# Optimization experiments

Hardware: AMD Instinct MI355X
Metric: run time of the kernel (lower is better)

## Reference

```python
import jax, jax.numpy as jnp
import numpy as np

N_NODES = 100000
N_EDGES = 3200000
IN_DIM = 512
HID = 256


def setup_inputs() -> dict:
    key = jax.random.key(0)
    ks = jax.random.split(key, 12)
    s1 = 1.0 / np.sqrt(HID)
    s2 = 1.0 / np.sqrt(HID)
    return {
        "inputs": jax.random.normal(ks[0], (N_NODES, IN_DIM), dtype=jnp.float32),
        "edge_rows": jax.random.randint(ks[1], (N_EDGES,), 0, N_NODES, dtype=jnp.int32),
        "edge_cols": jax.random.randint(ks[2], (N_EDGES,), 0, N_NODES, dtype=jnp.int32),
        "edge_vals": jax.random.uniform(ks[3], (N_EDGES,), dtype=jnp.float32),
        "W1": jax.random.uniform(ks[4], (IN_DIM, HID), minval=-s1, maxval=s1, dtype=jnp.float32),
        "b1": jax.random.uniform(ks[5], (HID,), minval=-s1, maxval=s1, dtype=jnp.float32),
        "W2": jax.random.uniform(ks[6], (HID, HID), minval=-s2, maxval=s2, dtype=jnp.float32),
        "b2": jax.random.uniform(ks[7], (HID,), minval=-s2, maxval=s2, dtype=jnp.float32),
        "fc1_W": jax.random.normal(ks[8], (HID, 32), dtype=jnp.float32) * 0.06,
        "fc1_b": jnp.zeros((32,), dtype=jnp.float32),
        "fc2_W": jax.random.normal(ks[9], (32, 2), dtype=jnp.float32) * 0.18,
        "fc2_b": jnp.zeros((2,), dtype=jnp.float32),
    }


def _spmm(rows, cols, vals, dense):
    # sparse[N,N] @ dense[N,D]: gather source rows, scale, scatter-add to dest rows
    gathered = dense[cols] * vals[:, None]          # [E, D]
    return jax.ops.segment_sum(gathered, rows, num_segments=N_NODES)


def _gcn_layer(x, rows, cols, vals, W, b):
    support = x @ W                                  # [N, out]
    return _spmm(rows, cols, vals, support) + b


def reference(inputs, edge_rows, edge_cols, edge_vals, W1, b1, W2, b2,
              fc1_W, fc1_b, fc2_W, fc2_b):
    h = jax.nn.relu(_gcn_layer(inputs, edge_rows, edge_cols, edge_vals, W1, b1))
    logits = _gcn_layer(h, edge_rows, edge_cols, edge_vals, W2, b2)
    h_a = jax.nn.relu(logits @ fc1_W + fc1_b)        # [N, 32]
    return jax.nn.log_softmax(h_a @ fc2_W + fc2_b, axis=1)  # [N, 2]
```

## Files before the change

kernel.cpp:

```cpp
#include <hip/hip_runtime.h>
#include <hip/hip_bf16.h>
#include <math.h>

#define N_NODES 100000
#define N_EDGES 3200000
#define IN_DIM  512
#define HID     256

#define NBUK    1021
#define ROWS_PBK 98
#define BCAPG   4096
#define CHUNK   4096
#define WFT_S   260

typedef __attribute__((ext_vector_type(8))) _Float16 f16x8;
typedef __attribute__((ext_vector_type(2))) _Float16 h2v;
typedef __attribute__((ext_vector_type(4))) float f32x4;

__device__ __forceinline__ ushort f2h(float f) {
  return __builtin_bit_cast(ushort, (_Float16)f);
}
__device__ __forceinline__ float hlo(uint u) {
  return (float)__builtin_bit_cast(h2v, u).x;
}
__device__ __forceinline__ float hhi(uint u) {
  return (float)__builtin_bit_cast(h2v, u).y;
}

__global__ __launch_bounds__(256) void fuse_weights(
    const float* __restrict__ W2, const float* __restrict__ fc1W,
    const float* __restrict__ b2, const float* __restrict__ fc1b,
    ushort* __restrict__ WfTb, float* __restrict__ bf,
    int* __restrict__ gcur) {
  int tid = threadIdx.x;
  int i = blockIdx.x * 32 + (tid >> 3);
  int jg = (tid & 7) * 4;
  float4 acc = {0.f, 0.f, 0.f, 0.f};
  for (int k = 0; k < HID; k++) {
    float w = W2[i * HID + k];
    float4 f = *(const float4*)(fc1W + k * 32 + jg);
    acc.x += w * f.x; acc.y += w * f.y; acc.z += w * f.z; acc.w += w * f.w;
  }
  WfTb[(jg + 0) * HID + i] = f2h(acc.x);
  WfTb[(jg + 1) * HID + i] = f2h(acc.y);
  WfTb[(jg + 2) * HID + i] = f2h(acc.z);
  WfTb[(jg + 3) * HID + i] = f2h(acc.w);
  if (blockIdx.x == 0 && tid < 32) {
    float s = fc1b[tid];
    for (int k = 0; k < HID; k++) s += b2[k] * fc1W[k * 32 + tid];
    bf[tid] = s;
  }
  int gid = blockIdx.x * 256 + tid;
  if (gid < NBUK) gcur[gid] = gid * BCAPG;
}

__global__ __launch_bounds__(256) void prep_w1t(
    const float* __restrict__ W1, ushort* __restrict__ W1T) {
  int n = blockIdx.x;
  for (int k = threadIdx.x; k < IN_DIM; k += 256)
    W1T[(size_t)n * IN_DIM + k] = f2h(W1[(size_t)k * HID + n]);
}

__global__ __launch_bounds__(256) void blocksum_kernel(
    const int* __restrict__ cnt, int* __restrict__ bsum, int n) {
  int i = blockIdx.x * 256 + threadIdx.x;
  int v = (i < n) ? cnt[i] : 0;
  #pragma unroll
  for (int m = 1; m < 64; m <<= 1) v += __shfl_xor(v, m, 64);
  __shared__ int ws[4];
  if ((threadIdx.x & 63) == 0) ws[threadIdx.x >> 6] = v;
  __syncthreads();
  if (threadIdx.x == 0) bsum[blockIdx.x] = ws[0] + ws[1] + ws[2] + ws[3];
}

__global__ __launch_bounds__(512) void scanpart_kernel(
    int* __restrict__ bsum, int nb) {
  int tid = threadIdx.x, lane = tid & 63, wid = tid >> 6;
  int v = (tid < nb) ? bsum[tid] : 0;
  int x = v;
  #pragma unroll
  for (int d = 1; d < 64; d <<= 1) {
    int y = __shfl_up(x, d, 64);
    if (lane >= d) x += y;
  }
  __shared__ int ws[8];
  if (lane == 63) ws[wid] = x;
  __syncthreads();
  int woff = 0;
  for (int w = 0; w < wid; w++) woff += ws[w];
  if (tid < nb) bsum[tid] = woff + x - v;
}

__global__ __launch_bounds__(256) void scanfinal_kernel(
    const int* __restrict__ cnt, const int* __restrict__ bsum,
    int* __restrict__ rowptr, int n) {
  int tid = threadIdx.x, lane = tid & 63, wid = tid >> 6;
  int i = blockIdx.x * 256 + tid;
  int v = (i < n) ? cnt[i] : 0;
  int x = v;
  #pragma unroll
  for (int d = 1; d < 64; d <<= 1) {
    int y = __shfl_up(x, d, 64);
    if (lane >= d) x += y;
  }
  __shared__ int ws[4];
  if (lane == 63) ws[wid] = x;
  __syncthreads();
  int woff = bsum[blockIdx.x];
  for (int w = 0; w < wid; w++) woff += ws[w];
  int excl = woff + x - v;
  if (i < n) rowptr[i] = excl;
  if (i == 0) rowptr[n] = N_EDGES;
}

__global__ __launch_bounds__(256) void scatter_p1(
    const int* __restrict__ rows, const int* __restrict__ cols,
    const float* __restrict__ vals, int* __restrict__ gcur,
    int2* __restrict__ tcv, int* __restrict__ cnt, int n) {
  __shared__ int bcnt[NBUK];
  __shared__ int bcur[NBUK];
  int tid = threadIdx.x;
  int chunk0 = blockIdx.x * CHUNK;
  for (int i = tid; i < NBUK; i += 256) bcnt[i] = 0;
  __syncthreads();

  int r[16], c[16], b[16];
  float v[16];
  #pragma unroll
  for (int i = 0; i < 16; i++) {
    int idx = chunk0 + i * 256 + tid;
    if (idx < n) {
      r[i] = rows[idx];
      c[i] = cols[idx];
      v[i] = vals[idx];
      b[i] = r[i] / ROWS_PBK;
      atomicAdd(&bcnt[b[i]], 1);
      atomicAdd(&cnt[r[i]], 1);
    } else {
      b[i] = -1;
    }
  }
  __syncthreads();
  for (int i = tid; i < NBUK; i += 256)
    if (bcnt[i] > 0) bcur[i] = atomicAdd(&gcur[i], bcnt[i]);
  __syncthreads();
  #pragma unroll
  for (int i = 0; i < 16; i++) {
    if (b[i] >= 0) {
      int p = atomicAdd(&bcur[b[i]], 1);
      int rl = r[i] - b[i] * ROWS_PBK;
      int2 e; e.x = (rl << 17) | c[i]; e.y = __float_as_int(v[i]);
      tcv[p] = e;
    }
  }
}

__global__ __launch_bounds__(256) void scatter_p2(
    const int* __restrict__ rowptr, const int2* __restrict__ tcv,
    int2* __restrict__ cv) {
  __shared__ int2 buf[BCAPG];
  __shared__ int lcur[ROWS_PBK];
  int b = blockIdx.x;
  int tid = threadIdx.x;
  int lo = b * ROWS_PBK;
  int hi = min(N_NODES, lo + ROWS_PBK);
  int nr = hi - lo;
  int base = rowptr[lo];
  int ecnt = rowptr[hi] - base;
  for (int r = tid; r < nr; r += 256) lcur[r] = rowptr[lo + r] - base;
  __syncthreads();
  const int2* src = tcv + (size_t)b * BCAPG;
  for (int i = tid; i < ecnt; i += 256) {
    int2 e = src[i];
    int rl = ((uint)e.x) >> 17;
    int p = atomicAdd(&lcur[rl], 1);
    int2 o; o.x = e.x & 0x1FFFF; o.y = e.y;
    buf[p] = o;
  }
  __syncthreads();
  int2* dst = cv + base;
  for (int i = tid; i < ecnt; i += 256) dst[i] = buf[i];
}

__global__ __launch_bounds__(512, 4) void gemm1_mfma(
    const float* __restrict__ A, const ushort* __restrict__ BT,
    ushort* __restrict__ C, int M) {
  __shared__ __align__(16) char smem[32768];
  ushort* As = (ushort*)smem;
  ushort* Bs = (ushort*)(smem + 10240);
  int tid = threadIdx.x;
  int bm = blockIdx.x * 128;
  int lane = tid & 63, wid = tid >> 6;
  int waveM = wid >> 2, waveN = wid & 3;
  int l16 = lane & 15, quad = lane >> 4;

  f32x4 acc[4][4] = {};

  int ar = tid >> 2;
  int ac = (tid & 3) * 8;
  const float* aptr = A + (size_t)(bm + ar) * IN_DIM + ac;
  bool avalid = (bm + ar) < M;
  ushort* aw = As + ar * 40 + ac;
  int br = tid >> 1;
  int bc = (tid & 1) * 16;
  const ushort* bptr = BT + (size_t)br * IN_DIM + bc;
  ushort* bw = Bs + br * 40 + bc;

  for (int k0 = 0; k0 < IN_DIM; k0 += 32) {
    #pragma unroll
    for (int i = 0; i < 2; i++) {
      float4 av = {0.f, 0.f, 0.f, 0.f};
      if (avalid) av = *(const float4*)(aptr + k0 + i * 4);
      ushort4 p;
      p.x = f2h(av.x); p.y = f2h(av.y); p.z = f2h(av.z); p.w = f2h(av.w);
      *(ushort4*)(aw + i * 4) = p;
    }
    *(int4*)bw = *(const int4*)(bptr + k0);
    *(int4*)(bw + 8) = *(const int4*)(bptr + k0 + 8);
    __syncthreads();

    f16x8 af[4], bfv[4];
    #pragma unroll
    for (int mi = 0; mi < 4; mi++)
      af[mi] = *(const f16x8*)(As + (waveM * 64 + mi * 16 + l16) * 40 + quad * 8);
    #pragma unroll
    for (int ni = 0; ni < 4; ni++)
      bfv[ni] = *(const f16x8*)(Bs + (waveN * 64 + ni * 16 + l16) * 40 + quad * 8);
    #pragma unroll
    for (int mi = 0; mi < 4; mi++)
      #pragma unroll
      for (int ni = 0; ni < 4; ni++)
        acc[mi][ni] = __builtin_amdgcn_mfma_f32_16x16x32_f16(
            af[mi], bfv[ni], acc[mi][ni], 0, 0, 0);
    __syncthreads();
  }

  ushort* Cs = (ushort*)smem;
  #pragma unroll
  for (int wm = 0; wm < 2; wm++) {
    if (waveM == wm) {
      #pragma unroll
      for (int mi = 0; mi < 4; mi++)
        #pragma unroll
        for (int ni = 0; ni < 4; ni++)
          #pragma unroll
          for (int r = 0; r < 4; r++)
            Cs[(mi * 16 + quad * 4 + r) * 256 + waveN * 64 + ni * 16 + l16] =
                f2h(acc[mi][ni][r]);
    }
    __syncthreads();
    int rbase = bm + wm * 64;
    #pragma unroll
    for (int i = 0; i < 4; i++) {
      int f = tid + i * 512;
      int r = f >> 5, v8 = f & 31;
      if (rbase + r < M)
        *(int4*)(C + (size_t)(rbase + r) * HID + v8 * 8) =
            *(const int4*)(Cs + r * 256 + v8 * 8);
    }
    __syncthreads();
  }
}

__global__ __launch_bounds__(512, 8) void spmm_fused(
    const int* __restrict__ rowptr, const int2* __restrict__ cv,
    const ushort* __restrict__ S, const float* __restrict__ bias,
    const ushort* __restrict__ WfTb, ushort* __restrict__ S2b, int nrows) {
  __shared__ ushort WfT[32 * WFT_S];
  __shared__ float hbuf[8][256];
  int tid = threadIdx.x;
  for (int idx = tid; idx < 32 * 64; idx += 512) {
    int jj = idx >> 6, kg = idx & 63;
    *(ushort4*)&WfT[jj * WFT_S + kg * 4] = *(const ushort4*)&WfTb[jj * HID + kg * 4];
  }
  __syncthreads();

  int w = tid >> 6, lane = tid & 63;
  int row = blockIdx.x * 8 + w;
  if (row >= nrows) return;
  int start = rowptr[row], end = rowptr[row + 1];
  float A0 = 0.f, A1 = 0.f, A2 = 0.f, A3 = 0.f;
  const ushort* Sl = S + lane * 4;
  int j = start;
  if ((j & 1) && j < end) {
    int2 e0 = cv[j];
    float v0 = __int_as_float(e0.y);
    uint2 u0 = *(const uint2*)(Sl + (size_t)e0.x * HID);
    A0 += v0 * hlo(u0.x); A1 += v0 * hhi(u0.x);
    A2 += v0 * hlo(u0.y); A3 += v0 * hhi(u0.y);
    j++;
  }
  for (; j + 7 < end; j += 8) {
    int4 E[4];
    #pragma unroll
    for (int t = 0; t < 4; t++)
      E[t] = *(const int4*)((const int*)(cv + j) + t * 4);
    uint2 u[8];
    #pragma unroll
    for (int t = 0; t < 4; t++) {
      u[2 * t]     = *(const uint2*)(Sl + (size_t)E[t].x * HID);
      u[2 * t + 1] = *(const uint2*)(Sl + (size_t)E[t].z * HID);
    }
    #pragma unroll
    for (int t = 0; t < 4; t++) {
      float va = __int_as_float(E[t].y);
      float vb = __int_as_float(E[t].w);
      A0 += va * hlo(u[2 * t].x);     A1 += va * hhi(u[2 * t].x);
      A2 += va * hlo(u[2 * t].y);     A3 += va * hhi(u[2 * t].y);
      A0 += vb * hlo(u[2 * t + 1].x); A1 += vb * hhi(u[2 * t + 1].x);
      A2 += vb * hlo(u[2 * t + 1].y); A3 += vb * hhi(u[2 * t + 1].y);
    }
  }
  for (; j + 1 < end; j += 2) {
    int4 E = *(const int4*)(cv + j);
    uint2 ua = *(const uint2*)(Sl + (size_t)E.x * HID);
    uint2 ub = *(const uint2*)(Sl + (size_t)E.z * HID);
    float va = __int_as_float(E.y), vb = __int_as_float(E.w);
    A0 += va * hlo(ua.x); A1 += va * hhi(ua.x);
    A2 += va * hlo(ua.y); A3 += va * hhi(ua.y);
    A0 += vb * hlo(ub.x); A1 += vb * hhi(ub.x);
    A2 += vb * hlo(ub.y); A3 += vb * hhi(ub.y);
  }
  if (j < end) {
    int2 e0 = cv[j];
    float v0 = __int_as_float(e0.y);
    uint2 u0 = *(const uint2*)(Sl + (size_t)e0.x * HID);
    A0 += v0 * hlo(u0.x); A1 += v0 * hhi(u0.x);
    A2 += v0 * hlo(u0.y); A3 += v0 * hhi(u0.y);
  }
  float4 b = *(const float4*)(bias + lane * 4);
  float4 h;
  h.x = fmaxf(A0 + b.x, 0.f);
  h.y = fmaxf(A1 + b.y, 0.f);
  h.z = fmaxf(A2 + b.z, 0.f);
  h.w = fmaxf(A3 + b.w, 0.f);
  *(float4*)(&hbuf[w][lane * 4]) = h;

  int jo = lane & 31;
  int kbase = (lane >> 5) * 128;
  const float* hb = &hbuf[w][kbase];
  const ushort* wt = &WfT[jo * WFT_S + kbase];
  float c0 = 0.f, c1 = 0.f, c2 = 0.f, c3 = 0.f;
  #pragma unroll
  for (int kk = 0; kk < 32; kk++) {
    float4 hv = *(const float4*)(hb + kk * 4);
    uint2 wv = *(const uint2*)(wt + kk * 4);
    c0 += hv.x * hlo(wv.x); c1 += hv.y * hhi(wv.x);
    c2 += hv.z * hlo(wv.y); c3 += hv.w * hhi(wv.y);
  }
  float acc = (c0 + c1) + (c2 + c3);
  acc += __shfl_xor(acc, 32, 64);
  if (lane < 32) S2b[(size_t)row * 32 + jo] = f2h(acc);
}

__global__ __launch_bounds__(256) void spmm32_out_kernel(
    const int* __restrict__ rowptr, const int2* __restrict__ cv,
    const ushort* __restrict__ S2b, const float* __restrict__ bf,
    const float* __restrict__ fc2W, const float* __restrict__ fc2b,
    float* __restrict__ out, int nrows) {
  int sub = threadIdx.x >> 4;
  int l16 = threadIdx.x & 15;
  int row = blockIdx.x * 16 + sub;
  if (row >= nrows) return;
  int start = rowptr[row], end = rowptr[row + 1];
  float a0 = 0.f, a1 = 0.f;
  const ushort* Sl = S2b + l16 * 2;
  int j = start;
  if ((j & 1) && j < end) {
    int2 e0 = cv[j];
    float v0 = __int_as_float(e0.y);
    uint u0 = *(const uint*)(Sl + (size_t)e0.x * 32);
    a0 += v0 * hlo(u0); a1 += v0 * hhi(u0);
    j++;
  }
  for (; j + 15 < end; j += 16) {
    int4 E[8];
    #pragma unroll
    for (int t = 0; t < 8; t++)
      E[t] = *(const int4*)((const int*)(cv + j) + t * 4);
    uint u[16];
    #pragma unroll
    for (int t = 0; t < 8; t++) {
      u[2 * t]     = *(const uint*)(Sl + (size_t)E[t].x * 32);
      u[2 * t + 1] = *(const uint*)(Sl + (size_t)E[t].z * 32);
    }
    #pragma unroll
    for (int t = 0; t < 8; t++) {
      float va = __int_as_float(E[t].y);
      float vb = __int_as_float(E[t].w);
      a0 += va * hlo(u[2 * t]);     a1 += va * hhi(u[2 * t]);
      a0 += vb * hlo(u[2 * t + 1]); a1 += vb * hhi(u[2 * t + 1]);
    }
  }
  for (; j + 1 < end; j += 2) {
    int4 E = *(const int4*)(cv + j);
    uint ua = *(const uint*)(Sl + (size_t)E.x * 32);
    uint ub = *(const uint*)(Sl + (size_t)E.z * 32);
    float va = __int_as_float(E.y), vb = __int_as_float(E.w);
    a0 += va * hlo(ua); a1 += va * hhi(ua);
    a0 += vb * hlo(ub); a1 += vb * hhi(ub);
  }
  if (j < end) {
    int2 e0 = cv[j];
    float v0 = __int_as_float(e0.y);
    uint u0 = *(const uint*)(Sl + (size_t)e0.x * 32);
    a0 += v0 * hlo(u0); a1 += v0 * hhi(u0);
  }
  int k0 = l16 * 2, k1 = l16 * 2 + 1;
  float h0 = fmaxf(a0 + bf[k0], 0.f);
  float h1 = fmaxf(a1 + bf[k1], 0.f);
  float z0p = h0 * fc2W[k0 * 2 + 0] + h1 * fc2W[k1 * 2 + 0];
  float z1p = h0 * fc2W[k0 * 2 + 1] + h1 * fc2W[k1 * 2 + 1];
  #pragma unroll
  for (int m = 8; m >= 1; m >>= 1) {
    z0p += __shfl_xor(z0p, m, 16);
    z1p += __shfl_xor(z1p, m, 16);
  }
  if (l16 == 0) {
    float z0 = z0p + fc2b[0];
    float z1 = z1p + fc2b[1];
    float mx = fmaxf(z0, z1);
    float lse = mx + logf(expf(z0 - mx) + expf(z1 - mx));
    float2 o = {z0 - lse, z1 - lse};
    *(float2*)(out + (size_t)row * 2) = o;
  }
}

extern "C" void kernel_launch(void* const* d_in, const int* in_sizes, int n_in,
                              void* d_out, int out_size, void* d_ws, size_t ws_size,
                              hipStream_t stream) {
  const float* X     = (const float*)d_in[0];
  const int*   erow  = (const int*)d_in[1];
  const int*   ecol  = (const int*)d_in[2];
  const float* eval_ = (const float*)d_in[3];
  const float* W1    = (const float*)d_in[4];
  const float* b1    = (const float*)d_in[5];
  const float* W2    = (const float*)d_in[6];
  const float* b2    = (const float*)d_in[7];
  const float* fc1W  = (const float*)d_in[8];
  const float* fc1b  = (const float*)d_in[9];
  const float* fc2W  = (const float*)d_in[10];
  const float* fc2b  = (const float*)d_in[11];
  float* out = (float*)d_out;

  size_t off = 0;
  auto alloc = [&](size_t bytes) {
    void* p = (char*)d_ws + off;
    off += (bytes + 255) & ~(size_t)255;
    return p;
  };
  ushort* WfTb   = (ushort*)alloc((size_t)HID * 32 * 2);
  float*  bf     = (float*)alloc(32 * 4);
  int*    cnt    = (int*)alloc((size_t)N_NODES * 4);
  int*    rowptr = (int*)alloc((size_t)(N_NODES + 1) * 4);
  int*    bsum   = (int*)alloc((size_t)512 * 4);
  int*    gcur   = (int*)alloc((size_t)NBUK * 4);
  int2*   cv     = (int2*)alloc((size_t)N_EDGES * 8);
  int2*   tcv    = (int2*)alloc((size_t)NBUK * BCAPG * 8);
  ushort* W1T    = (ushort*)alloc((size_t)HID * IN_DIM * 2);
  ushort* S1b    = (ushort*)alloc((size_t)N_NODES * HID * 2);
  ushort* S2b    = (ushort*)alloc((size_t)N_NODES * 32 * 2);
  (void)ws_size; (void)n_in; (void)in_sizes; (void)out_size;

  const int NBLK = (N_NODES + 255) / 256;
  const int NCHUNK = (N_EDGES + CHUNK - 1) / CHUNK;

  hipMemsetAsync(cnt, 0, (size_t)N_NODES * 4, stream);

  fuse_weights<<<8, 256, 0, stream>>>(W2, fc1W, b2, fc1b, WfTb, bf, gcur);
  prep_w1t<<<HID, 256, 0, stream>>>(W1, W1T);

  scatter_p1<<<NCHUNK, 256, 0, stream>>>(
      erow, ecol, eval_, gcur, tcv, cnt, N_EDGES);
  blocksum_kernel<<<NBLK, 256, 0, stream>>>(cnt, bsum, N_NODES);
  scanpart_kernel<<<1, 512, 0, stream>>>(bsum, NBLK);
  scanfinal_kernel<<<NBLK, 256, 0, stream>>>(cnt, bsum, rowptr, N_NODES);
  scatter_p2<<<NBUK, 256, 0, stream>>>(rowptr, tcv, cv);

  gemm1_mfma<<<(N_NODES + 127) / 128, 512, 0, stream>>>(X, W1T, S1b, N_NODES);

  spmm_fused<<<(N_NODES + 7) / 8, 512, 0, stream>>>(
      rowptr, cv, S1b, b1, WfTb, S2b, N_NODES);

  spmm32_out_kernel<<<(N_NODES + 15) / 16, 256, 0, stream>>>(
      rowptr, cv, S2b, bf, fc2W, fc2b, out, N_NODES);
}
```

Before: 812.1 us.

## Derive CSR rowptr from bucket counts, drop global per-row count atomics and scans

Stops counting edges per row with global atomics in scatter_p1. Row offsets are now computed from per-bucket totals: a single-block scan over the 1021 buckets, then a per-bucket count-and-scan in shared memory inside scatter_p2. This removes the memset, the 3.2M global atomics and three scan kernels, in exchange for an extra pass over the bucket's edges in scatter_p2. It also splits spmm_fused into two launches over row halves, which adds a launch and has no clear speed purpose.

```diff
diff --git a/kernel.cpp b/kernel.cpp
--- a/kernel.cpp
+++ b/kernel.cpp
@@ -12,6 +12,7 @@
 #define BCAPG   4096
 #define CHUNK   4096
 #define WFT_S   260
+#define SPMM_HALF 50000
 
 typedef __attribute__((ext_vector_type(8))) _Float16 f16x8;
 typedef __attribute__((ext_vector_type(2))) _Float16 h2v;
@@ -61,62 +62,10 @@
     W1T[(size_t)n * IN_DIM + k] = f2h(W1[(size_t)k * HID + n]);
 }
 
-__global__ __launch_bounds__(256) void blocksum_kernel(
-    const int* __restrict__ cnt, int* __restrict__ bsum, int n) {
-  int i = blockIdx.x * 256 + threadIdx.x;
-  int v = (i < n) ? cnt[i] : 0;
-  #pragma unroll
-  for (int m = 1; m < 64; m <<= 1) v += __shfl_xor(v, m, 64);
-  __shared__ int ws[4];
-  if ((threadIdx.x & 63) == 0) ws[threadIdx.x >> 6] = v;
-  __syncthreads();
-  if (threadIdx.x == 0) bsum[blockIdx.x] = ws[0] + ws[1] + ws[2] + ws[3];
-}
-
-__global__ __launch_bounds__(512) void scanpart_kernel(
-    int* __restrict__ bsum, int nb) {
-  int tid = threadIdx.x, lane = tid & 63, wid = tid >> 6;
-  int v = (tid < nb) ? bsum[tid] : 0;
-  int x = v;
-  #pragma unroll
-  for (int d = 1; d < 64; d <<= 1) {
-    int y = __shfl_up(x, d, 64);
-    if (lane >= d) x += y;
-  }
-  __shared__ int ws[8];
-  if (lane == 63) ws[wid] = x;
-  __syncthreads();
-  int woff = 0;
-  for (int w = 0; w < wid; w++) woff += ws[w];
-  if (tid < nb) bsum[tid] = woff + x - v;
-}
-
-__global__ __launch_bounds__(256) void scanfinal_kernel(
-    const int* __restrict__ cnt, const int* __restrict__ bsum,
-    int* __restrict__ rowptr, int n) {
-  int tid = threadIdx.x, lane = tid & 63, wid = tid >> 6;
-  int i = blockIdx.x * 256 + tid;
-  int v = (i < n) ? cnt[i] : 0;
-  int x = v;
-  #pragma unroll
-  for (int d = 1; d < 64; d <<= 1) {
-    int y = __shfl_up(x, d, 64);
-    if (lane >= d) x += y;
-  }
-  __shared__ int ws[4];
-  if (lane == 63) ws[wid] = x;
-  __syncthreads();
-  int woff = bsum[blockIdx.x];
-  for (int w = 0; w < wid; w++) woff += ws[w];
-  int excl = woff + x - v;
-  if (i < n) rowptr[i] = excl;
-  if (i == 0) rowptr[n] = N_EDGES;
-}
-
 __global__ __launch_bounds__(256) void scatter_p1(
     const int* __restrict__ rows, const int* __restrict__ cols,
     const float* __restrict__ vals, int* __restrict__ gcur,
-    int2* __restrict__ tcv, int* __restrict__ cnt, int n) {
+    int2* __restrict__ tcv, int n) {
   __shared__ int bcnt[NBUK];
   __shared__ int bcur[NBUK];
   int tid = threadIdx.x;
@@ -135,7 +84,6 @@
       v[i] = vals[idx];
       b[i] = r[i] / ROWS_PBK;
       atomicAdd(&bcnt[b[i]], 1);
-      atomicAdd(&cnt[r[i]], 1);
     } else {
       b[i] = -1;
     }
@@ -155,21 +103,68 @@
   }
 }
 
+__global__ __launch_bounds__(1024) void bukscan(
+    const int* __restrict__ gcur, int* __restrict__ bbase,
+    int* __restrict__ rowptr) {
+  int tid = threadIdx.x, lane = tid & 63, wid = tid >> 6;
+  int v = (tid < NBUK) ? (gcur[tid] - tid * BCAPG) : 0;
+  int x = v;
+  #pragma unroll
+  for (int d = 1; d < 64; d <<= 1) {
+    int y = __shfl_up(x, d, 64);
+    if (lane >= d) x += y;
+  }
+  __shared__ int ws[16];
+  if (lane == 63) ws[wid] = x;
+  __syncthreads();
+  int woff = 0;
+  for (int w = 0; w < wid; w++) woff += ws[w];
+  if (tid < NBUK) bbase[tid] = woff + x - v;
+  if (tid == 0) { bbase[NBUK] = N_EDGES; rowptr[N_NODES] = N_EDGES; }
+}
+
 __global__ __launch_bounds__(256) void scatter_p2(
-    const int* __restrict__ rowptr, const int2* __restrict__ tcv,
-    int2* __restrict__ cv) {
+    const int* __restrict__ bbase, const int2* __restrict__ tcv,
+    int* __restrict__ rowptr, int2* __restrict__ cv) {
   __shared__ int2 buf[BCAPG];
+  __shared__ int rcnt[ROWS_PBK];
   __shared__ int lcur[ROWS_PBK];
+  __shared__ int ws[4];
   int b = blockIdx.x;
   int tid = threadIdx.x;
   int lo = b * ROWS_PBK;
   int hi = min(N_NODES, lo + ROWS_PBK);
   int nr = hi - lo;
-  int base = rowptr[lo];
-  int ecnt = rowptr[hi] - base;
-  for (int r = tid; r < nr; r += 256) lcur[r] = rowptr[lo + r] - base;
+  int base = bbase[b];
+  int ecnt = bbase[b + 1] - base;
+  for (int r = tid; r < nr; r += 256) rcnt[r] = 0;
   __syncthreads();
   const int2* src = tcv + (size_t)b * BCAPG;
+  for (int i = tid; i < ecnt; i += 256) {
+    int2 e = src[i];
+    atomicAdd(&rcnt[((uint)e.x) >> 17], 1);
+  }
+  __syncthreads();
+  {
+    int lane = tid & 63, wid = tid >> 6;
+    int v = (tid < nr) ? rcnt[tid] : 0;
+    int x = v;
+    #pragma unroll
+    for (int d = 1; d < 64; d <<= 1) {
+      int y = __shfl_up(x, d, 64);
+      if (lane >= d) x += y;
+    }
+    if (lane == 63) ws[wid] = x;
+    __syncthreads();
+    int woff = 0;
+    for (int w = 0; w < wid; w++) woff += ws[w];
+    if (tid < nr) {
+      int excl = woff + x - v;
+      lcur[tid] = excl;
+      rowptr[lo + tid] = base + excl;
+    }
+  }
+  __syncthreads();
   for (int i = tid; i < ecnt; i += 256) {
     int2 e = src[i];
     int rl = ((uint)e.x) >> 17;
@@ -265,7 +260,8 @@
 __global__ __launch_bounds__(512, 8) void spmm_fused(
     const int* __restrict__ rowptr, const int2* __restrict__ cv,
     const ushort* __restrict__ S, const float* __restrict__ bias,
-    const ushort* __restrict__ WfTb, ushort* __restrict__ S2b, int nrows) {
+    const ushort* __restrict__ WfTb, ushort* __restrict__ S2b,
+    int row0, int row1) {
   __shared__ ushort WfT[32 * WFT_S];
   __shared__ float hbuf[8][256];
   int tid = threadIdx.x;
@@ -276,8 +272,8 @@
   __syncthreads();
 
   int w = tid >> 6, lane = tid & 63;
-  int row = blockIdx.x * 8 + w;
-  if (row >= nrows) return;
+  int row = row0 + blockIdx.x * 8 + w;
+  if (row >= row1) return;
   int start = rowptr[row], end = rowptr[row + 1];
   float A0 = 0.f, A1 = 0.f, A2 = 0.f, A3 = 0.f;
   const ushort* Sl = S + lane * 4;
@@ -451,9 +447,8 @@
   };
   ushort* WfTb   = (ushort*)alloc((size_t)HID * 32 * 2);
   float*  bf     = (float*)alloc(32 * 4);
-  int*    cnt    = (int*)alloc((size_t)N_NODES * 4);
   int*    rowptr = (int*)alloc((size_t)(N_NODES + 1) * 4);
-  int*    bsum   = (int*)alloc((size_t)512 * 4);
+  int*    bbase  = (int*)alloc((size_t)(NBUK + 1) * 4);
   int*    gcur   = (int*)alloc((size_t)NBUK * 4);
   int2*   cv     = (int2*)alloc((size_t)N_EDGES * 8);
   int2*   tcv    = (int2*)alloc((size_t)NBUK * BCAPG * 8);
@@ -462,25 +457,21 @@
   ushort* S2b    = (ushort*)alloc((size_t)N_NODES * 32 * 2);
   (void)ws_size; (void)n_in; (void)in_sizes; (void)out_size;
 
-  const int NBLK = (N_NODES + 255) / 256;
   const int NCHUNK = (N_EDGES + CHUNK - 1) / CHUNK;
-
-  hipMemsetAsync(cnt, 0, (size_t)N_NODES * 4, stream);
 
   fuse_weights<<<8, 256, 0, stream>>>(W2, fc1W, b2, fc1b, WfTb, bf, gcur);
   prep_w1t<<<HID, 256, 0, stream>>>(W1, W1T);
 
-  scatter_p1<<<NCHUNK, 256, 0, stream>>>(
-      erow, ecol, eval_, gcur, tcv, cnt, N_EDGES);
-  blocksum_kernel<<<NBLK, 256, 0, stream>>>(cnt, bsum, N_NODES);
-  scanpart_kernel<<<1, 512, 0, stream>>>(bsum, NBLK);
-  scanfinal_kernel<<<NBLK, 256, 0, stream>>>(cnt, bsum, rowptr, N_NODES);
-  scatter_p2<<<NBUK, 256, 0, stream>>>(rowptr, tcv, cv);
+  scatter_p1<<<NCHUNK, 256, 0, stream>>>(erow, ecol, eval_, gcur, tcv, N_EDGES);
+  bukscan<<<1, 1024, 0, stream>>>(gcur, bbase, rowptr);
+  scatter_p2<<<NBUK, 256, 0, stream>>>(bbase, tcv, rowptr, cv);
 
   gemm1_mfma<<<(N_NODES + 127) / 128, 512, 0, stream>>>(X, W1T, S1b, N_NODES);
 
-  spmm_fused<<<(N_NODES + 7) / 8, 512, 0, stream>>>(
-      rowptr, cv, S1b, b1, WfTb, S2b, N_NODES);
+  spmm_fused<<<(SPMM_HALF + 7) / 8, 512, 0, stream>>>(
+      rowptr, cv, S1b, b1, WfTb, S2b, 0, SPMM_HALF);
+  spmm_fused<<<(N_NODES - SPMM_HALF + 7) / 8, 512, 0, stream>>>(
+      rowptr, cv, S1b, b1, WfTb, S2b, SPMM_HALF, N_NODES);
 
   spmm32_out_kernel<<<(N_NODES + 15) / 16, 256, 0, stream>>>(
       rowptr, cv, S2b, bf, fc2W, fc2b, out, N_NODES);
```

Result: faster. 709.3 us (-12.7%).
